# Performance work log

Measured on AMD Instinct MI355X. Metric: run time of the kernel, lower is better.

## Reference

```python
import jax, jax.numpy as jnp
import numpy as np

RADIUS = 0.2
NSAMPLE = 32


def setup_inputs() -> dict:
    key = jax.random.key(0)
    k1, k2 = jax.random.split(key)
    B, N = 8, 4096
    xyz = jax.random.uniform(k1, (B, N, 3), dtype=jnp.float32)
    xyz_new = jax.random.uniform(k2, (B, N, 3), dtype=jnp.float32)  # ignored by forward, kept for signature fidelity
    return {"xyz": xyz, "xyz_new": xyz_new}


def _ball_query(radius, nsample, xyz, new_xyz):
    # xyz: [B, N, 3] source points; new_xyz: [B, M, 3] query centers.
    # Returns idx: [B, M, nsample] int32, matching pointnet2 CUDA ball_query:
    # first `nsample` indices j (in increasing j order) with ||q - p_j||^2 < r^2;
    # unused slots are filled with the first valid index.
    B, N, _ = xyz.shape
    sq_src = jnp.sum(xyz * xyz, axis=-1)          # [B, N]
    sq_q = jnp.sum(new_xyz * new_xyz, axis=-1)    # [B, M]
    # d2[b, m, n] = ||q_m - p_n||^2
    d2 = sq_q[:, :, None] + sq_src[:, None, :] - 2.0 * jnp.einsum(
        "bmc,bnc->bmn", new_xyz, xyz)             # [B, M, N]
    mask = d2 < (radius * radius)                 # [B, M, N] bool
    # key = index j when within radius, else sentinel N (sorts to the end)
    idx_range = jnp.arange(N, dtype=jnp.int32)
    keys = jnp.where(mask, idx_range[None, None, :], jnp.int32(N))
    sorted_keys = jnp.sort(keys, axis=-1)[..., :nsample]  # [B, M, nsample]
    first = sorted_keys[..., 0:1]                 # first valid index (pad value)
    idx = jnp.where(sorted_keys < N, sorted_keys, first)
    return idx.astype(jnp.int32)


def reference(xyz, xyz_new):
    # Faithful to the module: ball_query(radius, nsample, xyz, xyz) — xyz_new unused.
    return _ball_query(RADIUS, NSAMPLE, xyz, xyz)
```

## Files before the change

kernel.cpp:

```cpp
#include <hip/hip_runtime.h>
#include <cstdint>


#define BQ_N    4096
#define BQ_B    8
#define BQ_NS   32
#define BQ_R2   0.04f
#define BQ_NC   16

__device__ __forceinline__ float sq_plain(float x, float y, float z) {
    float r, t;
    asm("v_mul_f32 %0, %2, %2\n\t"
        "v_mul_f32 %1, %3, %3\n\t"
        "v_add_f32 %0, %0, %1\n\t"
        "v_mul_f32 %1, %4, %4\n\t"
        "v_add_f32 %0, %0, %1"
        : "=&v"(r), "=&v"(t)
        : "v"(x), "v"(y), "v"(z));
    return r;
}

__device__ __forceinline__ float d2_mixed(float qx, float qy, float qz, float sqq,
                                          float sx, float sy, float sz, float sqs) {
    float r, t;
    asm("v_mul_f32 %0, %2, %5\n\t"
        "v_fma_f32 %0, %3, %6, %0\n\t"
        "v_fma_f32 %0, %4, %7, %0\n\t"
        "v_add_f32 %0, %0, %0\n\t"
        "v_add_f32 %1, %8, %9\n\t"
        "v_sub_f32 %0, %1, %0"
        : "=&v"(r), "=&v"(t)
        : "v"(qx), "v"(qy), "v"(qz), "v"(sx), "v"(sy), "v"(sz),
          "v"(sqq), "v"(sqs));
    return r;
}

__device__ __forceinline__ int rfl(int v) {
    return __builtin_amdgcn_readfirstlane(v);
}

__device__ __forceinline__ void loadc(const float* __restrict__ src, int lane,
                                      int c, float X[4], float Y[4], float Z[4])
{
    #pragma unroll
    for (int u = 0; u < 4; ++u) {
        const int k = (c << 2) + u;
        const float* p = src + (size_t)(((k << 6) + lane) * 3);
        X[u] = p[0]; Y[u] = p[1]; Z[u] = p[2];
    }
}

__device__ __forceinline__ void procc(const float X[4], const float Y[4],
                                      const float Z[4], int lane, int c,
                                      const float4 Q[8], uint64_t W[8],
                                      int P[8], int F[8])
{
    float SQ[4];
    #pragma unroll
    for (int u = 0; u < 4; ++u) SQ[u] = sq_plain(X[u], Y[u], Z[u]);

    #pragma unroll
    for (int j = 0; j < 8; ++j) {
        if (rfl(F[j]) < BQ_NS) {
            #pragma unroll
            for (int u = 0; u < 4; ++u) {
                const int k = (c << 2) + u;
                const float d2 = d2_mixed(Q[j].x, Q[j].y, Q[j].z, Q[j].w,
                                          X[u], Y[u], Z[u], SQ[u]);
                const uint64_t bal = __ballot(d2 < BQ_R2);
                if (lane == k) { W[j] = bal; P[j] = F[j]; }
                F[j] += (int)__popcll(bal);
            }
        }
    }
}

__device__ __forceinline__ bool alldone(const int F[8]) {
    int m = F[0];
    #pragma unroll
    for (int j = 1; j < 8; ++j) m = min(m, F[j]);
    return rfl(m) >= BQ_NS;
}

__device__ __forceinline__ void emit_query(int* __restrict__ orow, int lane,
                                           uint64_t word, int wpre, int total)
{
    uint64_t w = word;
    int pos = wpre;
    while (w != 0ull && pos < BQ_NS) {
        const int bit = __builtin_ctzll(w);
        orow[pos] = (lane << 6) + bit;
        w &= (w - 1);
        ++pos;
    }
    if (total < BQ_NS) {
        int first;
        const uint64_t nz = __ballot(word != 0ull);
        if (nz == 0ull) {
            first = BQ_N;
        } else {
            const int fl = __builtin_ctzll(nz);
            const uint64_t fw = __shfl(word, fl);
            first = (fl << 6) + __builtin_ctzll(fw);
        }
        if (lane >= total && lane < BQ_NS) orow[lane] = first;
    }
}

__global__ __launch_bounds__(128, 4)
void ball_query_kernel(const float* __restrict__ xyz, int* __restrict__ out)
{
    const int b    = blockIdx.x >> 8;
    const int wq   = ((blockIdx.x & 255) << 4) + ((threadIdx.x >> 6) << 3);
    const int lane = threadIdx.x & 63;
    const float* __restrict__ src = xyz + (size_t)b * BQ_N * 3;
    int* __restrict__ outb = out + (size_t)(b * BQ_N) * BQ_NS;

    float4 Q[8];
    #pragma unroll
    for (int j = 0; j < 8; ++j) {
        const int m = wq + j;
        const float x = src[3 * m + 0];
        const float y = src[3 * m + 1];
        const float z = src[3 * m + 2];
        Q[j] = make_float4(x, y, z, sq_plain(x, y, z));
    }

    uint64_t W[8] = {0, 0, 0, 0, 0, 0, 0, 0};
    int      P[8] = {0, 0, 0, 0, 0, 0, 0, 0};
    int      F[8] = {0, 0, 0, 0, 0, 0, 0, 0};

    float XA[4], YA[4], ZA[4], XB[4], YB[4], ZB[4];
    loadc(src, lane, 0, XA, YA, ZA);

    int c = 0;
    for (;;) {
        int cn = (c + 1 < BQ_NC) ? c + 1 : c;
        loadc(src, lane, cn, XB, YB, ZB);
        procc(XA, YA, ZA, lane, c, Q, W, P, F);
        ++c;
        if (c >= BQ_NC || alldone(F)) break;

        cn = (c + 1 < BQ_NC) ? c + 1 : c;
        loadc(src, lane, cn, XA, YA, ZA);
        procc(XB, YB, ZB, lane, c, Q, W, P, F);
        ++c;
        if (c >= BQ_NC || alldone(F)) break;
    }

    #pragma unroll
    for (int j = 0; j < 8; ++j)
        emit_query(outb + (size_t)(wq + j) * BQ_NS, lane, W[j], P[j], F[j]);
}

extern "C" void kernel_launch(void* const* d_in, const int* in_sizes, int n_in,
                              void* d_out, int out_size, void* d_ws, size_t ws_size,
                              hipStream_t stream)
{
    const float* xyz = (const float*)d_in[0];
    int* out = (int*)d_out;
    hipLaunchKernelGGL(ball_query_kernel, dim3(2048), dim3(128), 0, stream,
                       xyz, out);
}
```

Baseline: 79.67 us.

## Use packed FP32 math for distance tests and drop manual double-buffered loads

Distance computation now uses v_pk_mul/fma/add_f32 so two source points are evaluated per instruction per query. The explicit A/B register double-buffering of source coordinates is replaced by a simple loop with per-iteration loads. The readfirstlane calls on the early-exit checks are removed, leaving uniformity to the compiler. Packed math cuts VALU instruction count, but losing the explicit prefetch may expose load latency, and the per-element extraction of d2 for the ballots adds overhead.

```diff
diff --git a/kernel.cpp b/kernel.cpp
--- a/kernel.cpp
+++ b/kernel.cpp
@@ -7,6 +7,8 @@
 #define BQ_NS   32
 #define BQ_R2   0.04f
 #define BQ_NC   16
+
+typedef float v2f __attribute__((ext_vector_type(2)));
 
 __device__ __forceinline__ float sq_plain(float x, float y, float z) {
     float r, t;
@@ -20,71 +22,50 @@
     return r;
 }
 
-__device__ __forceinline__ float d2_mixed(float qx, float qy, float qz, float sqq,
-                                          float sx, float sy, float sz, float sqs) {
-    float r, t;
-    asm("v_mul_f32 %0, %2, %5\n\t"
-        "v_fma_f32 %0, %3, %6, %0\n\t"
-        "v_fma_f32 %0, %4, %7, %0\n\t"
-        "v_add_f32 %0, %0, %0\n\t"
-        "v_add_f32 %1, %8, %9\n\t"
-        "v_sub_f32 %0, %1, %0"
+__device__ __forceinline__ v2f sq2_plain(v2f x, v2f y, v2f z) {
+    v2f r, t;
+    asm("v_pk_mul_f32 %0, %2, %2 op_sel:[0,0] op_sel_hi:[1,1]\n\t"
+        "v_pk_mul_f32 %1, %3, %3 op_sel:[0,0] op_sel_hi:[1,1]\n\t"
+        "v_pk_add_f32 %0, %0, %1 op_sel:[0,0] op_sel_hi:[1,1]\n\t"
+        "v_pk_mul_f32 %1, %4, %4 op_sel:[0,0] op_sel_hi:[1,1]\n\t"
+        "v_pk_add_f32 %0, %0, %1 op_sel:[0,0] op_sel_hi:[1,1]"
         : "=&v"(r), "=&v"(t)
-        : "v"(qx), "v"(qy), "v"(qz), "v"(sx), "v"(sy), "v"(sz),
-          "v"(sqq), "v"(sqs));
+        : "v"(x), "v"(y), "v"(z));
     return r;
 }
 
-__device__ __forceinline__ int rfl(int v) {
-    return __builtin_amdgcn_readfirstlane(v);
+__device__ __forceinline__ v2f d2_pk(v2f qa, v2f qb, v2f sx, v2f sy, v2f sz,
+                                     v2f sq2) {
+    v2f r, t;
+    asm("v_pk_mul_f32 %0, %2, %4 op_sel:[0,0] op_sel_hi:[0,1]\n\t"
+        "v_pk_fma_f32 %0, %2, %5, %0 op_sel:[1,0,0] op_sel_hi:[1,1,1]\n\t"
+        "v_pk_fma_f32 %0, %3, %6, %0 op_sel:[0,0,0] op_sel_hi:[0,1,1]\n\t"
+        "v_pk_add_f32 %0, %0, %0 op_sel:[0,0] op_sel_hi:[1,1]\n\t"
+        "v_pk_add_f32 %1, %3, %7 op_sel:[1,0] op_sel_hi:[1,1]\n\t"
+        "v_pk_add_f32 %0, %1, %0 op_sel:[0,0] op_sel_hi:[1,1] neg_lo:[0,1] neg_hi:[0,1]"
+        : "=&v"(r), "=&v"(t)
+        : "v"(qa), "v"(qb), "v"(sx), "v"(sy), "v"(sz), "v"(sq2));
+    return r;
 }
 
-__device__ __forceinline__ void loadc(const float* __restrict__ src, int lane,
-                                      int c, float X[4], float Y[4], float Z[4])
-{
-    #pragma unroll
-    for (int u = 0; u < 4; ++u) {
-        const int k = (c << 2) + u;
-        const float* p = src + (size_t)(((k << 6) + lane) * 3);
-        X[u] = p[0]; Y[u] = p[1]; Z[u] = p[2];
-    }
-}
-
-__device__ __forceinline__ void procc(const float X[4], const float Y[4],
-                                      const float Z[4], int lane, int c,
-                                      const float4 Q[8], uint64_t W[8],
-                                      int P[8], int F[8])
-{
-    float SQ[4];
-    #pragma unroll
-    for (int u = 0; u < 4; ++u) SQ[u] = sq_plain(X[u], Y[u], Z[u]);
-
-    #pragma unroll
-    for (int j = 0; j < 8; ++j) {
-        if (rfl(F[j]) < BQ_NS) {
-            #pragma unroll
-            for (int u = 0; u < 4; ++u) {
-                const int k = (c << 2) + u;
-                const float d2 = d2_mixed(Q[j].x, Q[j].y, Q[j].z, Q[j].w,
-                                          X[u], Y[u], Z[u], SQ[u]);
-                const uint64_t bal = __ballot(d2 < BQ_R2);
-                if (lane == k) { W[j] = bal; P[j] = F[j]; }
-                F[j] += (int)__popcll(bal);
-            }
-        }
-    }
-}
-
-__device__ __forceinline__ bool alldone(const int F[8]) {
-    int m = F[0];
-    #pragma unroll
-    for (int j = 1; j < 8; ++j) m = min(m, F[j]);
-    return rfl(m) >= BQ_NS;
+__device__ __forceinline__ void proc_pair(v2f qa, v2f qb, v2f sx, v2f sy,
+                                          v2f sz, v2f sq2, int lane, int k,
+                                          uint32_t& wlo, uint32_t& whi,
+                                          int& p, int& f) {
+    const v2f d2 = d2_pk(qa, qb, sx, sy, sz, sq2);
+    const uint64_t b0 = __ballot(d2[0] < BQ_R2);
+    if (lane == k)     { wlo = (uint32_t)b0; whi = (uint32_t)(b0 >> 32); p = f; }
+    f += (int)__popcll(b0);
+    const uint64_t b1 = __ballot(d2[1] < BQ_R2);
+    if (lane == k + 1) { wlo = (uint32_t)b1; whi = (uint32_t)(b1 >> 32); p = f; }
+    f += (int)__popcll(b1);
 }
 
 __device__ __forceinline__ void emit_query(int* __restrict__ orow, int lane,
-                                           uint64_t word, int wpre, int total)
+                                           uint32_t wlo, uint32_t whi,
+                                           int wpre, int total)
 {
+    const uint64_t word = ((uint64_t)whi << 32) | wlo;
     uint64_t w = word;
     int pos = wpre;
     while (w != 0ull && pos < BQ_NS) {
@@ -116,41 +97,58 @@
     const float* __restrict__ src = xyz + (size_t)b * BQ_N * 3;
     int* __restrict__ outb = out + (size_t)(b * BQ_N) * BQ_NS;
 
-    float4 Q[8];
+    v2f Qa[8], Qb[8];
     #pragma unroll
     for (int j = 0; j < 8; ++j) {
         const int m = wq + j;
         const float x = src[3 * m + 0];
         const float y = src[3 * m + 1];
         const float z = src[3 * m + 2];
-        Q[j] = make_float4(x, y, z, sq_plain(x, y, z));
+        Qa[j][0] = x; Qa[j][1] = y;
+        Qb[j][0] = z; Qb[j][1] = sq_plain(x, y, z);
     }
 
-    uint64_t W[8] = {0, 0, 0, 0, 0, 0, 0, 0};
-    int      P[8] = {0, 0, 0, 0, 0, 0, 0, 0};
-    int      F[8] = {0, 0, 0, 0, 0, 0, 0, 0};
+    uint32_t Wlo[8] = {0,0,0,0,0,0,0,0};
+    uint32_t Whi[8] = {0,0,0,0,0,0,0,0};
+    int      P[8]   = {0,0,0,0,0,0,0,0};
+    int      F[8]   = {0,0,0,0,0,0,0,0};
 
-    float XA[4], YA[4], ZA[4], XB[4], YB[4], ZB[4];
-    loadc(src, lane, 0, XA, YA, ZA);
+    const float* lp = src + lane * 3;
 
-    int c = 0;
-    for (;;) {
-        int cn = (c + 1 < BQ_NC) ? c + 1 : c;
-        loadc(src, lane, cn, XB, YB, ZB);
-        procc(XA, YA, ZA, lane, c, Q, W, P, F);
-        ++c;
-        if (c >= BQ_NC || alldone(F)) break;
+    for (int c = 0; c < BQ_NC; ++c) {
+        v2f X01, Y01, Z01, X23, Y23, Z23;
+        X01[0] = lp[  0]; X01[1] = lp[192];
+        Y01[0] = lp[  1]; Y01[1] = lp[193];
+        Z01[0] = lp[  2]; Z01[1] = lp[194];
+        X23[0] = lp[384]; X23[1] = lp[576];
+        Y23[0] = lp[385]; Y23[1] = lp[577];
+        Z23[0] = lp[386]; Z23[1] = lp[578];
+        lp += 768;
 
-        cn = (c + 1 < BQ_NC) ? c + 1 : c;
-        loadc(src, lane, cn, XA, YA, ZA);
-        procc(XB, YB, ZB, lane, c, Q, W, P, F);
-        ++c;
-        if (c >= BQ_NC || alldone(F)) break;
+        const v2f SQ01 = sq2_plain(X01, Y01, Z01);
+        const v2f SQ23 = sq2_plain(X23, Y23, Z23);
+
+        const int k0 = c << 2;
+        #pragma unroll
+        for (int j = 0; j < 8; ++j) {
+            if (F[j] < BQ_NS) {
+                proc_pair(Qa[j], Qb[j], X01, Y01, Z01, SQ01, lane, k0,
+                          Wlo[j], Whi[j], P[j], F[j]);
+                proc_pair(Qa[j], Qb[j], X23, Y23, Z23, SQ23, lane, k0 + 2,
+                          Wlo[j], Whi[j], P[j], F[j]);
+            }
+        }
+
+        int m = F[0];
+        #pragma unroll
+        for (int j = 1; j < 8; ++j) m = min(m, F[j]);
+        if (m >= BQ_NS) break;
     }
 
     #pragma unroll
     for (int j = 0; j < 8; ++j)
-        emit_query(outb + (size_t)(wq + j) * BQ_NS, lane, W[j], P[j], F[j]);
+        emit_query(outb + (size_t)(wq + j) * BQ_NS, lane,
+                   Wlo[j], Whi[j], P[j], F[j]);
 }
 
 extern "C" void kernel_launch(void* const* d_in, const int* in_sizes, int n_in,
```

Measured after the change: 80.37 us. About the same (+0.9%).
